# Optimization experiments

Measured on AMD Instinct MI355X. Metric: run time of the kernel, lower is better.

Reference implementation:

```python
import jax, jax.numpy as jnp
import numpy as np

GRID = 7  # hardcoded 7x7 spatial grid in the source -> seq len 49
H, DK, DV = 8, 64, 64
DILATE_P = 1


def _dilate_mask(p=DILATE_P):
    # indexes: (2, 49) of (row, col) coords of the 7x7 grid (torch.meshgrid 'ij')
    i, j = jnp.meshgrid(jnp.arange(GRID), jnp.arange(GRID), indexing='ij')
    idx = jnp.stack([i.flatten(), j.flatten()])  # (2, 49)
    diff = jnp.abs(idx.T[:, :, None] - idx[None])  # (49, 2, 49)
    cheb = diff.max(axis=1)   # Chebyshev distance (49, 49)
    manh = diff.sum(axis=1)   # Manhattan distance (49, 49)
    R = (cheb == p) & ((manh == p) | (manh == 2 * p))
    return R.astype(jnp.float32)


def setup_inputs() -> dict:
    key = jax.random.key(0)
    ks = jax.random.split(key, 8)
    B, N, D = 2048, GRID * GRID, 512
    s = 1.0 / np.sqrt(D)
    return {
        'queries': jax.random.normal(ks[0], (B, N, D), jnp.float32),
        'keys':    jax.random.normal(ks[1], (B, N, D), jnp.float32),
        'values':  jax.random.normal(ks[2], (B, N, D), jnp.float32),
        'Wq': jax.random.normal(ks[3], (H * DK, D), jnp.float32) * s,
        'bq': jnp.zeros((H * DK,), jnp.float32),
        'Wk': jax.random.normal(ks[4], (H * DK, D), jnp.float32) * s,
        'bk': jnp.zeros((H * DK,), jnp.float32),
        'Wv': jax.random.normal(ks[5], (H * DV, D), jnp.float32) * s,
        'bv': jnp.zeros((H * DV,), jnp.float32),
        'Wo': jax.random.normal(ks[6], (D // 8, H * DV), jnp.float32) * s,
        'bo': jnp.zeros((D // 8,), jnp.float32),
    }


def reference(queries, keys, values, Wq, bq, Wk, bk, Wv, bv, Wo, bo):
    b, nq, _ = queries.shape
    nk = keys.shape[1]
    mask = _dilate_mask()  # (nq, nk) 0/1 float
    # projections -> (b, h, n, d)
    q = (queries @ Wq.T + bq).reshape(b, nq, H, DK).transpose(0, 2, 1, 3)
    k = (keys @ Wk.T + bk).reshape(b, nk, H, DK).transpose(0, 2, 1, 3)
    v = (values @ Wv.T + bv).reshape(b, nk, H, DV).transpose(0, 2, 1, 3)
    # QK^T, multiplicative dilated mask (zeros, NOT -inf), then scale & softmax
    att = jnp.einsum('bhqd,bhkd->bhqk', q, k)
    att = att * mask / np.sqrt(DK)
    att = jax.nn.softmax(att, axis=-1)  # dropout is identity in eval
    out = jnp.einsum('bhqk,bhkd->bhqd', att, v)
    out = out.transpose(0, 2, 1, 3).reshape(b, nq, H * DV)
    return out @ Wo.T + bo
```

## Files before the change

kernel.cpp:

```cpp
#include <hip/hip_runtime.h>


#define MTOT 100352

typedef float f32x4 __attribute__((ext_vector_type(4)));
typedef __bf16 bf16x8 __attribute__((ext_vector_type(8)));
typedef unsigned short us8v __attribute__((ext_vector_type(8)));

__device__ __forceinline__ unsigned short f2bf(float f) {
    unsigned int u = __float_as_uint(f);
    u += 0x7fffu + ((u >> 16) & 1u);
    return (unsigned short)(u >> 16);
}

__device__ __forceinline__ bf16x8 ld_frag(const unsigned short* p) {
    us8v r = *(const us8v*)p;
    return __builtin_bit_cast(bf16x8, r);
}

__device__ __forceinline__ f32x4 mfma16(bf16x8 a, bf16x8 b, f32x4 c) {
    return __builtin_amdgcn_mfma_f32_16x16x32_bf16(a, b, c, 0, 0, 0);
}

__global__ __launch_bounds__(256) void proj_gemm(
    const float* __restrict__ Xq, const float* __restrict__ Xk, const float* __restrict__ Xv,
    const float* __restrict__ Wq, const float* __restrict__ Wk, const float* __restrict__ Wv,
    const float* __restrict__ bq, const float* __restrict__ bk, const float* __restrict__ bv,
    unsigned short* __restrict__ outbase)
{
    const int s = blockIdx.z;
    const float* X    = (s == 0) ? Xq : (s == 1) ? Xk : Xv;
    const float* W    = (s == 0) ? Wq : (s == 1) ? Wk : Wv;
    const float* bias = (s == 0) ? bq : (s == 1) ? bk : bv;
    unsigned short* out = outbase + (size_t)s * MTOT * 512;

    const int mbase = blockIdx.y * 128;
    const int nbase = blockIdx.x * 128;

    __shared__ __align__(16) unsigned short smA[128 * 72];
    __shared__ __align__(16) unsigned short smB[128 * 72];

    const int tid  = threadIdx.x;
    const int wave = tid >> 6, lane = tid & 63;
    const int lm   = lane & 15, quad = lane >> 4;
    const int wm   = (wave & 1) * 64, wn = (wave >> 1) * 64;

    f32x4 acc[4][4];
#pragma unroll
    for (int i = 0; i < 4; i++)
#pragma unroll
        for (int j = 0; j < 4; j++) acc[i][j] = (f32x4){0.f, 0.f, 0.f, 0.f};

    for (int k0 = 0; k0 < 512; k0 += 64) {
#pragma unroll
        for (int i = 0; i < 8; i++) {
            int f   = tid + 256 * i;
            int row = f >> 4;
            int c4  = (f & 15) * 4;
            float4 av = *(const float4*)(X + (size_t)(mbase + row) * 512 + k0 + c4);
            ushort4 wa;
            wa.x = f2bf(av.x); wa.y = f2bf(av.y); wa.z = f2bf(av.z); wa.w = f2bf(av.w);
            *(ushort4*)(smA + row * 72 + c4) = wa;
            float4 bv4 = *(const float4*)(W + (size_t)(nbase + row) * 512 + k0 + c4);
            ushort4 wb;
            wb.x = f2bf(bv4.x); wb.y = f2bf(bv4.y); wb.z = f2bf(bv4.z); wb.w = f2bf(bv4.w);
            *(ushort4*)(smB + row * 72 + c4) = wb;
        }
        __syncthreads();
#pragma unroll
        for (int kk = 0; kk < 64; kk += 32) {
            bf16x8 af[4], bfr[4];
#pragma unroll
            for (int mi = 0; mi < 4; mi++)
                af[mi] = ld_frag(smA + (wm + mi * 16 + lm) * 72 + kk + quad * 8);
#pragma unroll
            for (int ni = 0; ni < 4; ni++)
                bfr[ni] = ld_frag(smB + (wn + ni * 16 + lm) * 72 + kk + quad * 8);
#pragma unroll
            for (int mi = 0; mi < 4; mi++)
#pragma unroll
                for (int ni = 0; ni < 4; ni++)
                    acc[mi][ni] = mfma16(af[mi], bfr[ni], acc[mi][ni]);
        }
        __syncthreads();
    }

#pragma unroll
    for (int mi = 0; mi < 4; mi++) {
#pragma unroll
        for (int ni = 0; ni < 4; ni++) {
            int n = nbase + wn + ni * 16 + lm;
            float bb = bias[n];
#pragma unroll
            for (int r = 0; r < 4; r++) {
                int m = mbase + wm + mi * 16 + quad * 4 + r;
                out[(size_t)m * 512 + n] = f2bf(acc[mi][ni][r] + bb);
            }
        }
    }
}

__global__ __launch_bounds__(256) void attn_fused(
    const unsigned short* __restrict__ qkv,
    const float* __restrict__ Wo, const float* __restrict__ bo,
    float* __restrict__ out)
{
    const int b   = blockIdx.x;
    const int tid = threadIdx.x;
    const int wave = tid >> 6, lane = tid & 63;
    const int lm = lane & 15, quad = lane >> 4;

    const size_t QK = (size_t)MTOT * 512;
    const unsigned short* qg = qkv;
    const unsigned short* kg = qkv + QK;
    const unsigned short* vg = qkv + 2 * QK;
    const size_t brow = (size_t)b * 49;

    __shared__ __align__(16) unsigned short qb[64 * 72];
    __shared__ __align__(16) unsigned short kb[64 * 72];
    __shared__ __align__(16) unsigned short vT[64 * 72];
    __shared__ __align__(16) unsigned short Wos[64 * 72];
    __shared__ __align__(16) float Sb[64 * 68];

    f32x4 oacc[4];
#pragma unroll
    for (int i = 0; i < 4; i++) oacc[i] = (f32x4){0.f, 0.f, 0.f, 0.f};

    for (int h = 0; h < 8; h++) {
        __syncthreads();

#pragma unroll
        for (int i = 0; i < 4; i++) {
            int f = tid + 256 * i;
            if (f < 784) {
                int row = f >> 4, c = (f & 15) * 4;
                size_t src = (brow + row) * 512 + h * 64 + c;
                *(ushort4*)(qb + row * 72 + c) = *(const ushort4*)(qg + src);
                *(ushort4*)(kb + row * 72 + c) = *(const ushort4*)(kg + src);
            }
        }
#pragma unroll
        for (int i = 0; i < 13; i++) {
            int f = tid + 256 * i;
            if (f < 3136) {
                int row = f >> 6, d = f & 63;
                vT[d * 72 + row] = vg[(brow + row) * 512 + h * 64 + d];
            }
        }
        if (tid < 64) {
#pragma unroll
            for (int c = 49; c < 64; c++) vT[tid * 72 + c] = 0;
        }
#pragma unroll
        for (int i = 0; i < 4; i++) {
            int f = tid + 256 * i;
            int row = f >> 4, c = (f & 15) * 4;
            float4 wv = *(const float4*)(Wo + (size_t)row * 512 + h * 64 + c);
            ushort4 ww;
            ww.x = f2bf(wv.x); ww.y = f2bf(wv.y); ww.z = f2bf(wv.z); ww.w = f2bf(wv.w);
            *(ushort4*)(Wos + row * 72 + c) = ww;
        }
        __syncthreads();

        f32x4 sacc[4];
#pragma unroll
        for (int i = 0; i < 4; i++) sacc[i] = (f32x4){0.f, 0.f, 0.f, 0.f};
#pragma unroll
        for (int kk = 0; kk < 64; kk += 32) {
            bf16x8 af = ld_frag(qb + (16 * wave + lm) * 72 + kk + quad * 8);
#pragma unroll
            for (int ni = 0; ni < 4; ni++) {
                bf16x8 bf = ld_frag(kb + (ni * 16 + lm) * 72 + kk + quad * 8);
                sacc[ni] = mfma16(af, bf, sacc[ni]);
            }
        }
#pragma unroll
        for (int ni = 0; ni < 4; ni++)
#pragma unroll
            for (int r = 0; r < 4; r++)
                Sb[(16 * wave + quad * 4 + r) * 68 + ni * 16 + lm] = sacc[ni][r];
        __syncthreads();

        if (tid < 49) {
            int row = tid, ir = row / 7, ic = row % 7;
            float sum = 0.f;
            for (int j = 0; j < 49; j++) {
                int jr = j / 7, jc = j % 7;
                int dr = ir - jr; dr = dr < 0 ? -dr : dr;
                int dc = ic - jc; dc = dc < 0 ? -dc : dc;
                int ch = dr > dc ? dr : dc;
                float sv = (ch == 1) ? Sb[row * 68 + j] * 0.125f : 0.f;
                float e = __expf(sv);
                Sb[row * 68 + j] = e;
                sum += e;
            }
            float inv = 1.f / sum;
            for (int j = 0; j < 64; j++)
                qb[row * 72 + j] = (j < 49) ? f2bf(Sb[row * 68 + j] * inv)
                                            : (unsigned short)0;
        } else if (tid < 64) {
            for (int j = 0; j < 64; j++) qb[tid * 72 + j] = 0;
        }
        __syncthreads();

        f32x4 pacc[4];
#pragma unroll
        for (int i = 0; i < 4; i++) pacc[i] = (f32x4){0.f, 0.f, 0.f, 0.f};
#pragma unroll
        for (int kk = 0; kk < 64; kk += 32) {
            bf16x8 af = ld_frag(qb + (16 * wave + lm) * 72 + kk + quad * 8);
#pragma unroll
            for (int ni = 0; ni < 4; ni++) {
                bf16x8 bf = ld_frag(vT + (ni * 16 + lm) * 72 + kk + quad * 8);
                pacc[ni] = mfma16(af, bf, pacc[ni]);
            }
        }
#pragma unroll
        for (int ni = 0; ni < 4; ni++)
#pragma unroll
            for (int r = 0; r < 4; r++)
                kb[(16 * wave + quad * 4 + r) * 72 + ni * 16 + lm] = f2bf(pacc[ni][r]);
        __syncthreads();

#pragma unroll
        for (int kk = 0; kk < 64; kk += 32) {
            bf16x8 af = ld_frag(kb + (16 * wave + lm) * 72 + kk + quad * 8);
#pragma unroll
            for (int ni = 0; ni < 4; ni++) {
                bf16x8 bf = ld_frag(Wos + (ni * 16 + lm) * 72 + kk + quad * 8);
                oacc[ni] = mfma16(af, bf, oacc[ni]);
            }
        }
    }

#pragma unroll
    for (int ni = 0; ni < 4; ni++) {
        int n = ni * 16 + lm;
        float bb = bo[n];
#pragma unroll
        for (int r = 0; r < 4; r++) {
            int m = 16 * wave + quad * 4 + r;
            if (m < 49)
                out[(brow + m) * 64 + n] = oacc[ni][r] + bb;
        }
    }
}

extern "C" void kernel_launch(void* const* d_in, const int* in_sizes, int n_in,
                              void* d_out, int out_size, void* d_ws, size_t ws_size,
                              hipStream_t stream) {
    (void)in_sizes; (void)n_in; (void)out_size; (void)ws_size;
    const float* Xq = (const float*)d_in[0];
    const float* Xk = (const float*)d_in[1];
    const float* Xv = (const float*)d_in[2];
    const float* Wq = (const float*)d_in[3];
    const float* bq = (const float*)d_in[4];
    const float* Wk = (const float*)d_in[5];
    const float* bk = (const float*)d_in[6];
    const float* Wv = (const float*)d_in[7];
    const float* bv = (const float*)d_in[8];
    const float* Wo = (const float*)d_in[9];
    const float* bo = (const float*)d_in[10];

    unsigned short* qkv = (unsigned short*)d_ws;

    dim3 gA(4, 784, 3);
    proj_gemm<<<gA, dim3(256), 0, stream>>>(Xq, Xk, Xv, Wq, Wk, Wv, bq, bk, bv, qkv);
    attn_fused<<<dim3(2048), dim3(256), 0, stream>>>(qkv, Wo, bo, (float*)d_out);
}
```

Measured before the change: 1.264 ms.

## Pre-convert inputs to bf16 and use direct-to-LDS loads; register softmax in attention

Adds separate passes that convert X and W to bf16 in workspace, then a projection GEMM that loads tiles straight into LDS with global_load_lds and an XOR-swizzled layout. The weights are no longer re-read and re-converted per block. The attention kernel now does the masked softmax in registers with lane shuffles instead of a single-warp pass over shared memory, removing two barriers. It also vectorizes the V transpose loads and writes into a separate output buffer. The extra conversion pass adds a full read of the fp32 inputs plus a bf16 write and re-read, and needs a large workspace, with a fallback to the old path when the workspace is too small.

```diff
diff --git a/kernel.cpp b/kernel.cpp
--- a/kernel.cpp
+++ b/kernel.cpp
@@ -2,6 +2,8 @@
 
 
 #define MTOT 100352
+#define XN   51380224
+#define WN   262144
 
 typedef float f32x4 __attribute__((ext_vector_type(4)));
 typedef __bf16 bf16x8 __attribute__((ext_vector_type(8)));
@@ -12,17 +14,124 @@
     u += 0x7fffu + ((u >> 16) & 1u);
     return (unsigned short)(u >> 16);
 }
-
 __device__ __forceinline__ bf16x8 ld_frag(const unsigned short* p) {
     us8v r = *(const us8v*)p;
     return __builtin_bit_cast(bf16x8, r);
 }
-
 __device__ __forceinline__ f32x4 mfma16(bf16x8 a, bf16x8 b, f32x4 c) {
     return __builtin_amdgcn_mfma_f32_16x16x32_bf16(a, b, c, 0, 0, 0);
 }
-
-__global__ __launch_bounds__(256) void proj_gemm(
+__device__ __forceinline__ void glds16(const unsigned short* g, unsigned short* l) {
+    __builtin_amdgcn_global_load_lds(
+        (const __attribute__((address_space(1))) unsigned int*)g,
+        (__attribute__((address_space(3))) unsigned int*)l, 16, 0, 0);
+}
+
+__global__ __launch_bounds__(256) void cvt_x(
+    const float* __restrict__ x0, const float* __restrict__ x1, const float* __restrict__ x2,
+    unsigned short* __restrict__ dst)
+{
+    const float* src = (blockIdx.z == 0) ? x0 : (blockIdx.z == 1) ? x1 : x2;
+    unsigned short* d = dst + (size_t)blockIdx.z * XN;
+    const int n4 = XN / 4;
+    for (int i = blockIdx.x * 256 + threadIdx.x; i < n4; i += gridDim.x * 256) {
+        float4 v = ((const float4*)src)[i];
+        ushort4 o; o.x = f2bf(v.x); o.y = f2bf(v.y); o.z = f2bf(v.z); o.w = f2bf(v.w);
+        ((ushort4*)d)[i] = o;
+    }
+}
+
+__global__ __launch_bounds__(256) void cvt_w(
+    const float* __restrict__ w0, const float* __restrict__ w1, const float* __restrict__ w2,
+    unsigned short* __restrict__ dst)
+{
+    const float* src = (blockIdx.z == 0) ? w0 : (blockIdx.z == 1) ? w1 : w2;
+    unsigned short* d = dst + (size_t)blockIdx.z * WN;
+    const int n4 = WN / 4;
+    for (int i = blockIdx.x * 256 + threadIdx.x; i < n4; i += gridDim.x * 256) {
+        float4 v = ((const float4*)src)[i];
+        ushort4 o; o.x = f2bf(v.x); o.y = f2bf(v.y); o.z = f2bf(v.z); o.w = f2bf(v.w);
+        ((ushort4*)d)[i] = o;
+    }
+}
+
+__global__ __launch_bounds__(256) void proj_bf16(
+    const unsigned short* __restrict__ XB, const unsigned short* __restrict__ WB,
+    const float* __restrict__ bq, const float* __restrict__ bk, const float* __restrict__ bv,
+    unsigned short* __restrict__ qkv)
+{
+    const int s = blockIdx.z;
+    const unsigned short* X = XB + (size_t)s * XN;
+    const unsigned short* W = WB + (size_t)s * WN;
+    const float* bias = (s == 0) ? bq : (s == 1) ? bk : bv;
+    unsigned short* out = qkv + (size_t)s * XN;
+
+    const int mbase = blockIdx.y * 128;
+    const int nbase = blockIdx.x * 128;
+
+    __shared__ __align__(16) unsigned short smA[128 * 64];
+    __shared__ __align__(16) unsigned short smB[128 * 64];
+
+    const int tid = threadIdx.x;
+    const int wave = tid >> 6, lane = tid & 63;
+    const int lm = lane & 15, quad = lane >> 4;
+    const int wm = (wave & 1) * 64, wn = (wave >> 1) * 64;
+
+    const int l8 = lane >> 3;
+    const int cb = (lane & 7) ^ l8;
+    const unsigned short* gA = X + (size_t)(mbase + wave * 8 + l8) * 512 + cb * 8;
+    const unsigned short* gB = W + (size_t)(nbase + wave * 8 + l8) * 512 + cb * 8;
+    unsigned short* lA = smA + wave * 512;
+    unsigned short* lB = smB + wave * 512;
+
+    f32x4 acc[4][4];
+#pragma unroll
+    for (int i = 0; i < 4; i++)
+#pragma unroll
+        for (int jj = 0; jj < 4; jj++) acc[i][jj] = (f32x4){0.f, 0.f, 0.f, 0.f};
+
+    for (int k0 = 0; k0 < 512; k0 += 64) {
+#pragma unroll
+        for (int p = 0; p < 4; p++) {
+            glds16(gA + p * 32 * 512 + k0, lA + p * 2048);
+            glds16(gB + p * 32 * 512 + k0, lB + p * 2048);
+        }
+        __syncthreads();
+#pragma unroll
+        for (int kk8 = 0; kk8 <= 4; kk8 += 4) {
+            const int pb = ((kk8 + quad) ^ (lm & 7)) * 8;
+            bf16x8 af[4], bfr[4];
+#pragma unroll
+            for (int mi = 0; mi < 4; mi++)
+                af[mi] = ld_frag(smA + (wm + mi * 16 + lm) * 64 + pb);
+#pragma unroll
+            for (int ni = 0; ni < 4; ni++)
+                bfr[ni] = ld_frag(smB + (wn + ni * 16 + lm) * 64 + pb);
+#pragma unroll
+            for (int mi = 0; mi < 4; mi++)
+#pragma unroll
+                for (int ni = 0; ni < 4; ni++)
+                    acc[mi][ni] = mfma16(af[mi], bfr[ni], acc[mi][ni]);
+        }
+        __syncthreads();
+    }
+
+#pragma unroll
+    for (int ni = 0; ni < 4; ni++) {
+        int n = nbase + wn + ni * 16 + lm;
+        float bb = bias[n];
+#pragma unroll
+        for (int mi = 0; mi < 4; mi++) {
+#pragma unroll
+            for (int r = 0; r < 4; r++) {
+                int m = mbase + wm + mi * 16 + quad * 4 + r;
+                out[(size_t)m * 512 + n] = f2bf(acc[mi][ni][r] + bb);
+            }
+        }
+    }
+}
+
+__global__ __launch_bounds__(256) void proj_f32(
     const float* __restrict__ Xq, const float* __restrict__ Xk, const float* __restrict__ Xv,
     const float* __restrict__ Wq, const float* __restrict__ Wk, const float* __restrict__ Wv,
     const float* __restrict__ bq, const float* __restrict__ bk, const float* __restrict__ bv,
@@ -49,7 +158,7 @@
 #pragma unroll
     for (int i = 0; i < 4; i++)
 #pragma unroll
-        for (int j = 0; j < 4; j++) acc[i][j] = (f32x4){0.f, 0.f, 0.f, 0.f};
+        for (int jj = 0; jj < 4; jj++) acc[i][jj] = (f32x4){0.f, 0.f, 0.f, 0.f};
 
     for (int k0 = 0; k0 < 512; k0 += 64) {
 #pragma unroll
@@ -105,7 +214,7 @@
     const float* __restrict__ Wo, const float* __restrict__ bo,
     float* __restrict__ out)
 {
-    const int b   = blockIdx.x;
+    const int b = blockIdx.x;
     const int tid = threadIdx.x;
     const int wave = tid >> 6, lane = tid & 63;
     const int lm = lane & 15, quad = lane >> 4;
@@ -120,7 +229,23 @@
     __shared__ __align__(16) unsigned short kb[64 * 72];
     __shared__ __align__(16) unsigned short vT[64 * 72];
     __shared__ __align__(16) unsigned short Wos[64 * 72];
-    __shared__ __align__(16) float Sb[64 * 68];
+    __shared__ __align__(16) unsigned short ob[64 * 72];
+
+    int qrow[4], qir[4], qic[4];
+#pragma unroll
+    for (int r = 0; r < 4; r++) {
+        qrow[r] = 16 * wave + quad * 4 + r;
+        qir[r] = qrow[r] / 7;
+        qic[r] = qrow[r] - 7 * qir[r];
+    }
+    int jr[4], jc[4], jvalid[4];
+#pragma unroll
+    for (int ni = 0; ni < 4; ni++) {
+        int jj = ni * 16 + lm;
+        jvalid[ni] = (jj < 49);
+        jr[ni] = jj / 7;
+        jc[ni] = jj - 7 * jr[ni];
+    }
 
     f32x4 oacc[4];
 #pragma unroll
@@ -128,23 +253,28 @@
 
     for (int h = 0; h < 8; h++) {
         __syncthreads();
+        const int hoff = h * 64;
 
 #pragma unroll
         for (int i = 0; i < 4; i++) {
             int f = tid + 256 * i;
             if (f < 784) {
                 int row = f >> 4, c = (f & 15) * 4;
-                size_t src = (brow + row) * 512 + h * 64 + c;
+                size_t src = (brow + row) * 512 + hoff + c;
                 *(ushort4*)(qb + row * 72 + c) = *(const ushort4*)(qg + src);
                 *(ushort4*)(kb + row * 72 + c) = *(const ushort4*)(kg + src);
             }
         }
 #pragma unroll
-        for (int i = 0; i < 13; i++) {
+        for (int i = 0; i < 4; i++) {
             int f = tid + 256 * i;
-            if (f < 3136) {
-                int row = f >> 6, d = f & 63;
-                vT[d * 72 + row] = vg[(brow + row) * 512 + h * 64 + d];
+            if (f < 784) {
+                int row = f >> 4, c = (f & 15) * 4;
+                ushort4 vv = *(const ushort4*)(vg + (brow + row) * 512 + hoff + c);
+                vT[(c + 0) * 72 + row] = vv.x;
+                vT[(c + 1) * 72 + row] = vv.y;
+                vT[(c + 2) * 72 + row] = vv.z;
+                vT[(c + 3) * 72 + row] = vv.w;
             }
         }
         if (tid < 64) {
@@ -155,7 +285,7 @@
         for (int i = 0; i < 4; i++) {
             int f = tid + 256 * i;
             int row = f >> 4, c = (f & 15) * 4;
-            float4 wv = *(const float4*)(Wo + (size_t)row * 512 + h * 64 + c);
+            float4 wv = *(const float4*)(Wo + (size_t)row * 512 + hoff + c);
             ushort4 ww;
             ww.x = f2bf(wv.x); ww.y = f2bf(wv.y); ww.z = f2bf(wv.z); ww.w = f2bf(wv.w);
             *(ushort4*)(Wos + row * 72 + c) = ww;
@@ -169,39 +299,41 @@
         for (int kk = 0; kk < 64; kk += 32) {
             bf16x8 af = ld_frag(qb + (16 * wave + lm) * 72 + kk + quad * 8);
 #pragma unroll
-            for (int ni = 0; ni < 4; ni++) {
-                bf16x8 bf = ld_frag(kb + (ni * 16 + lm) * 72 + kk + quad * 8);
-                sacc[ni] = mfma16(af, bf, sacc[ni]);
+            for (int ni = 0; ni < 4; ni++)
+                sacc[ni] = mfma16(af, ld_frag(kb + (ni * 16 + lm) * 72 + kk + quad * 8), sacc[ni]);
+        }
+
+        float t[4] = {0.f, 0.f, 0.f, 0.f};
+#pragma unroll
+        for (int ni = 0; ni < 4; ni++) {
+#pragma unroll
+            for (int r = 0; r < 4; r++) {
+                float e = 0.f;
+                if (jvalid[ni] && qrow[r] < 49) {
+                    int dr = qir[r] - jr[ni]; dr = dr < 0 ? -dr : dr;
+                    int dc = qic[r] - jc[ni]; dc = dc < 0 ? -dc : dc;
+                    int ch = dr > dc ? dr : dc;
+                    float sv = (ch == 1) ? sacc[ni][r] * 0.125f : 0.f;
+                    e = __expf(sv);
+                }
+                sacc[ni][r] = e;
+                t[r] += e;
             }
         }
 #pragma unroll
+        for (int xm = 1; xm < 16; xm <<= 1) {
+#pragma unroll
+            for (int r = 0; r < 4; r++) t[r] += __shfl_xor(t[r], xm, 64);
+        }
+        float inv[4];
+#pragma unroll
+        for (int r = 0; r < 4; r++) inv[r] = (qrow[r] < 49) ? 1.f / t[r] : 0.f;
+
+#pragma unroll
         for (int ni = 0; ni < 4; ni++)
 #pragma unroll
             for (int r = 0; r < 4; r++)
-                Sb[(16 * wave + quad * 4 + r) * 68 + ni * 16 + lm] = sacc[ni][r];
-        __syncthreads();
-
-        if (tid < 49) {
-            int row = tid, ir = row / 7, ic = row % 7;
-            float sum = 0.f;
-            for (int j = 0; j < 49; j++) {
-                int jr = j / 7, jc = j % 7;
-                int dr = ir - jr; dr = dr < 0 ? -dr : dr;
-                int dc = ic - jc; dc = dc < 0 ? -dc : dc;
-                int ch = dr > dc ? dr : dc;
-                float sv = (ch == 1) ? Sb[row * 68 + j] * 0.125f : 0.f;
-                float e = __expf(sv);
-                Sb[row * 68 + j] = e;
-                sum += e;
-            }
-            float inv = 1.f / sum;
-            for (int j = 0; j < 64; j++)
-                qb[row * 72 + j] = (j < 49) ? f2bf(Sb[row * 68 + j] * inv)
-                                            : (unsigned short)0;
-        } else if (tid < 64) {
-            for (int j = 0; j < 64; j++) qb[tid * 72 + j] = 0;
-        }
-        __syncthreads();
+                qb[qrow[r] * 72 + ni * 16 + lm] = f2bf(sacc[ni][r] * inv[r]);
 
         f32x4 pacc[4];
 #pragma unroll
@@ -210,26 +342,21 @@
         for (int kk = 0; kk < 64; kk += 32) {
             bf16x8 af = ld_frag(qb + (16 * wave + lm) * 72 + kk + quad * 8);
 #pragma unroll
-            for (int ni = 0; ni < 4; ni++) {
-                bf16x8 bf = ld_frag(vT + (ni * 16 + lm) * 72 + kk + quad * 8);
-                pacc[ni] = mfma16(af, bf, pacc[ni]);
-            }
+            for (int ni = 0; ni < 4; ni++)
+                pacc[ni] = mfma16(af, ld_frag(vT + (ni * 16 + lm) * 72 + kk + quad * 8), pacc[ni]);
         }
 #pragma unroll
         for (int ni = 0; ni < 4; ni++)
 #pragma unroll
             for (int r = 0; r < 4; r++)
-                kb[(16 * wave + quad * 4 + r) * 72 + ni * 16 + lm] = f2bf(pacc[ni][r]);
-        __syncthreads();
+                ob[qrow[r] * 72 + ni * 16 + lm] = f2bf(pacc[ni][r]);
 
 #pragma unroll
         for (int kk = 0; kk < 64; kk += 32) {
-            bf16x8 af = ld_frag(kb + (16 * wave + lm) * 72 + kk + quad * 8);
-#pragma unroll
-            for (int ni = 0; ni < 4; ni++) {
-                bf16x8 bf = ld_frag(Wos + (ni * 16 + lm) * 72 + kk + quad * 8);
-                oacc[ni] = mfma16(af, bf, oacc[ni]);
-            }
+            bf16x8 af = ld_frag(ob + (16 * wave + lm) * 72 + kk + quad * 8);
+#pragma unroll
+            for (int ni = 0; ni < 4; ni++)
+                oacc[ni] = mfma16(af, ld_frag(Wos + (ni * 16 + lm) * 72 + kk + quad * 8), oacc[ni]);
         }
     }
 
@@ -238,18 +365,16 @@
         int n = ni * 16 + lm;
         float bb = bo[n];
 #pragma unroll
-        for (int r = 0; r < 4; r++) {
-            int m = 16 * wave + quad * 4 + r;
-            if (m < 49)
-                out[(brow + m) * 64 + n] = oacc[ni][r] + bb;
-        }
+        for (int r = 0; r < 4; r++)
+            if (qrow[r] < 49)
+                out[(brow + qrow[r]) * 64 + n] = oacc[ni][r] + bb;
     }
 }
 
 extern "C" void kernel_launch(void* const* d_in, const int* in_sizes, int n_in,
                               void* d_out, int out_size, void* d_ws, size_t ws_size,
                               hipStream_t stream) {
-    (void)in_sizes; (void)n_in; (void)out_size; (void)ws_size;
+    (void)in_sizes; (void)n_in; (void)out_size;
     const float* Xq = (const float*)d_in[0];
     const float* Xk = (const float*)d_in[1];
     const float* Xv = (const float*)d_in[2];
@@ -263,8 +388,17 @@
     const float* bo = (const float*)d_in[10];
 
     unsigned short* qkv = (unsigned short*)d_ws;
-
-    dim3 gA(4, 784, 3);
-    proj_gemm<<<gA, dim3(256), 0, stream>>>(Xq, Xk, Xv, Wq, Wk, Wv, bq, bk, bv, qkv);
+    const size_t NEED = ((size_t)6 * XN + 3 * WN) * 2;
+
+    if (ws_size >= NEED) {
+        unsigned short* XB = qkv + (size_t)3 * XN;
+        unsigned short* WB = XB + (size_t)3 * XN;
+        cvt_x<<<dim3(4096, 1, 3), 256, 0, stream>>>(Xq, Xk, Xv, XB);
+        cvt_w<<<dim3(64, 1, 3), 256, 0, stream>>>(Wq, Wk, Wv, WB);
+        proj_bf16<<<dim3(4, 784, 3), 256, 0, stream>>>(XB, WB, bq, bk, bv, qkv);
+    } else {
+        proj_f32<<<dim3(4, 784, 3), 256, 0, stream>>>(Xq, Xk, Xv, Wq, Wk, Wv,
+                                                      bq, bk, bv, qkv);
+    }
     attn_fused<<<dim3(2048), dim3(256), 0, stream>>>(qkv, Wo, bo, (float*)d_out);
 }
```

Result: faster. 1.041 ms (-17.6%).
